# Kernel optimization log

Hardware: AMD Instinct MI355X
Metric: run time of the kernel (lower is better)

Reference implementation:

```python
import jax, jax.numpy as jnp
import numpy as np

HARD_NUM = 700      # hardcoded self.hard_num in HardOIMLoss
OIM_SCALAR = 30.0   # oim_scalar init arg
N, D, P, Q = 4096, 256, 5532, 5000


def _l2norm(x):
    return x / jnp.linalg.norm(x, axis=-1, keepdims=True)


def setup_inputs() -> dict:
    key = jax.random.key(0)
    k1, k2, k3, k4, k5 = jax.random.split(key, 5)
    # OIM features and lookup tables are L2-normalized rows
    inputs = _l2norm(jax.random.normal(k1, (N, D), dtype=jnp.float32))
    lut = _l2norm(jax.random.normal(k2, (P, D), dtype=jnp.float32))
    cq = _l2norm(jax.random.normal(k3, (Q, D), dtype=jnp.float32))
    reliability = jax.random.uniform(k4, (P + Q,), dtype=jnp.float32)
    labels = jax.random.randint(k5, (N,), 0, P, dtype=jnp.int32)
    return {"inputs": inputs, "labels": labels, "lut": lut, "cq": cq,
            "reliability": reliability}


def reference(inputs, labels, lut, cq, reliability):
    # projected[n, c] = <inputs_n, table_c> * reliability_c ;  table = [lut; cq]
    table = jnp.concatenate([lut, cq], axis=0)            # [P+Q, D]
    projected = (inputs @ table.T) * reliability[None, :]  # [N, P+Q]
    C = projected.shape[1]
    # value at sorted-descending index HARD_NUM == (HARD_NUM+1)-th largest
    boundary = jax.lax.top_k(projected, HARD_NUM + 1)[0][:, -1]  # [N]
    hard_mask = projected >= boundary[:, None]
    label_mask = jnp.arange(C, dtype=labels.dtype)[None, :] == labels[:, None]
    mask = hard_mask | label_mask
    logits = jnp.where(mask, projected * OIM_SCALAR, -jnp.inf)
    # cross entropy (mean over rows); label column is always unmasked
    logZ = jax.scipy.special.logsumexp(logits, axis=1)
    tgt = jnp.take_along_axis(logits, labels[:, None].astype(jnp.int32), axis=1)[:, 0]
    return jnp.mean(logZ - tgt)
```

## Files before the change

### kernel.cpp

```cpp
#include <hip/hip_runtime.h>
#include <math.h>

#define N_ROWS 4096
#define DIM    256
#define P_SZ   5532
#define Q_SZ   5000
#define C_COLS 10532
#define TPAD   10624
#define PSTR   10624
#define NGR    (PSTR / 8)
#define NDW    (PSTR / 4)
#define K_SEL  701
#define SCALAR 30.0f
#define C2     (SCALAR * 1.4426950408889634f)

typedef __attribute__((ext_vector_type(8))) short   short8;
typedef __attribute__((ext_vector_type(4))) float   float4_t;
typedef __attribute__((ext_vector_type(4))) unsigned short ushort4_t;
typedef __attribute__((ext_vector_type(8))) unsigned short ushort8_t;
typedef __attribute__((ext_vector_type(4))) unsigned int  uint4_t;

__device__ __forceinline__ unsigned short f2bf(float f) {
    unsigned u = __float_as_uint(f);
    unsigned r = u + 0x7FFFu + ((u >> 16) & 1u);
    return (unsigned short)(r >> 16);
}
__device__ __forceinline__ float bf2f(unsigned short u) {
    return __uint_as_float((unsigned)u << 16);
}
__device__ __forceinline__ unsigned short key16(unsigned short u) {
    return (u & 0x8000u) ? (unsigned short)(~u) : (unsigned short)(u | 0x8000u);
}
__device__ __forceinline__ float key2f16(unsigned key) {
    unsigned short b = (key & 0x8000u) ? (unsigned short)(key & 0x7FFFu)
                                       : (unsigned short)(~key & 0xFFFFu);
    return bf2f(b);
}
__device__ __forceinline__ void gload16(const void* g, void* l) {
    __builtin_amdgcn_global_load_lds(
        (const __attribute__((address_space(1))) unsigned int*)g,
        (__attribute__((address_space(3))) unsigned int*)l, 16, 0, 0);
}

#define NIN_G  (N_ROWS * DIM / 4)
#define NTAB_G (TPAD * DIM / 4)

__global__ __launch_bounds__(256) void convert_bf16(
    const float* __restrict__ inputs, const float* __restrict__ lut,
    const float* __restrict__ cq, unsigned short* __restrict__ in_bf,
    unsigned short* __restrict__ tab_bf)
{
    const int g = blockIdx.x * 256 + threadIdx.x;
    if (g >= NIN_G + NTAB_G) return;
    float4_t v;
    unsigned short* dst;
    if (g < NIN_G) {
        v = *(const float4_t*)&inputs[(size_t)g * 4];
        dst = in_bf + (size_t)g * 4;
    } else {
        const int t = g - NIN_G;
        const int row = t >> 6;
        const int c4  = (t & 63) * 4;
        if (row < P_SZ)        v = *(const float4_t*)&lut[(size_t)row * DIM + c4];
        else if (row < C_COLS) v = *(const float4_t*)&cq[(size_t)(row - P_SZ) * DIM + c4];
        else                   v = (float4_t){0.f, 0.f, 0.f, 0.f};
        dst = tab_bf + (size_t)t * 4;
    }
    ushort4_t h = { f2bf(v.x), f2bf(v.y), f2bf(v.z), f2bf(v.w) };
    *(ushort4_t*)dst = h;
}

#define NWG_X 83
#define NWG_Y 32
#define NWG   (NWG_X * NWG_Y)
#define CSTR  132

__global__ __launch_bounds__(256) void gemm_proj(
    const unsigned short* __restrict__ in_bf,
    const unsigned short* __restrict__ tab_bf,
    const float* __restrict__ rel,
    unsigned short* __restrict__ proj)
{
    __shared__ __align__(16) unsigned short smem[128 * CSTR];
    unsigned short* At = smem;
    unsigned short* Bt = smem + 128 * 64;

    const int tid  = threadIdx.x;
    const int lane = tid & 63, wid = tid >> 6;
    const int wm = wid >> 1, wn = wid & 1;

    const int phys = blockIdx.x;
    const int wg   = (phys & 7) * (NWG / 8) + (phys >> 3);
    const int bx   = wg >> 5;
    const int by   = wg & 31;
    const int row0 = by * 128, col0 = bx * 128;

    float4_t acc[4][4];
    #pragma unroll
    for (int i = 0; i < 4; ++i)
        #pragma unroll
        for (int j = 0; j < 4; ++j)
            acc[i][j] = (float4_t){0.f, 0.f, 0.f, 0.f};

    for (int k0 = 0; k0 < DIM; k0 += 64) {
        #pragma unroll
        for (int it = 0; it < 4; ++it) {
            const int g  = it * 256 + tid;
            const int r  = g >> 3;
            const int kb = ((g & 7) * 16) ^ ((r & 7) << 4);
            gload16(in_bf  + (size_t)(row0 + r) * DIM + k0 + (kb >> 1),
                    (char*)At + g * 16);
            gload16(tab_bf + (size_t)(col0 + r) * DIM + k0 + (kb >> 1),
                    (char*)Bt + g * 16);
        }
        __syncthreads();

        #pragma unroll
        for (int kk = 0; kk < 2; ++kk) {
            const int krow = lane & 15;
            const int kb   = kk * 64 + ((lane >> 4) << 4);
            short8 af[4], bfr[4];
            #pragma unroll
            for (int i = 0; i < 4; ++i) {
                const int r = wm * 64 + i * 16 + krow;
                af[i] = *(const short8*)((const char*)At + (r * 128 + (kb ^ ((r & 7) << 4))));
            }
            #pragma unroll
            for (int j = 0; j < 4; ++j) {
                const int r = wn * 64 + j * 16 + krow;
                bfr[j] = *(const short8*)((const char*)Bt + (r * 128 + (kb ^ ((r & 7) << 4))));
            }
            #pragma unroll
            for (int i = 0; i < 4; ++i)
                #pragma unroll
                for (int j = 0; j < 4; ++j)
                    acc[i][j] = __builtin_amdgcn_mfma_f32_16x16x32_bf16(af[i], bfr[j], acc[i][j], 0, 0, 0);
        }
        __syncthreads();
    }

    const int lr = (lane >> 4) << 2;
    const int lc = lane & 15;
    #pragma unroll
    for (int j = 0; j < 4; ++j) {
        const int cl  = wn * 64 + j * 16 + lc;
        const int col = col0 + cl;
        const bool pad = (col >= C_COLS);
        const float rl = pad ? 0.f : rel[col];
        #pragma unroll
        for (int i = 0; i < 4; ++i) {
            const int rbase = wm * 64 + i * 16 + lr;
            #pragma unroll
            for (int rr = 0; rr < 4; ++rr)
                smem[(rbase + rr) * CSTR + cl] =
                    pad ? (unsigned short)0u : key16(f2bf(acc[i][j][rr] * rl));
        }
    }
    __syncthreads();
    #pragma unroll
    for (int it = 0; it < 8; ++it) {
        const int g = it * 256 + tid;
        const int r = g >> 4;
        const int c8 = (g & 15) * 8;
        *(ushort8_t*)(proj + (size_t)(row0 + r) * PSTR + col0 + c8) =
            *(const ushort8_t*)&smem[r * CSTR + c8];
    }
}

#define NCPY 16
__global__ __launch_bounds__(256) void row_loss_kernel(
    const unsigned short* __restrict__ proj, const int* __restrict__ labels,
    float* __restrict__ row_loss)
{
    __shared__ unsigned h1[NCPY * 257];
    __shared__ unsigned h2[256];
    __shared__ unsigned wsum[4];
    __shared__ float    fsum[4];
    __shared__ unsigned sel_bin, sel_k, sel_sub;

    const int tid = threadIdx.x, lane = tid & 63, wid = tid >> 6;
    const int row = blockIdx.x;
    const uint4_t* prow = (const uint4_t*)(proj + (size_t)row * PSTR);
    const unsigned cbase = (unsigned)(tid & (NCPY - 1)) * 257;

    for (int i = tid; i < NCPY * 257; i += 256) h1[i] = 0;
    if (tid < 256) h2[tid] = 0;
    __syncthreads();

    #pragma unroll
    for (int it = 0; it < 5; ++it) {
        const uint4_t w = prow[it * 256 + tid];
        #pragma unroll
        for (int d = 0; d < 4; ++d) {
            atomicAdd(&h1[cbase + ((w[d] >> 8) & 0xFFu)], 1u);
            atomicAdd(&h1[cbase + (w[d] >> 24)], 1u);
        }
    }
    if (tid < NGR - 1280) {
        const uint4_t w = prow[1280 + tid];
        #pragma unroll
        for (int d = 0; d < 4; ++d) {
            atomicAdd(&h1[cbase + ((w[d] >> 8) & 0xFFu)], 1u);
            atomicAdd(&h1[cbase + (w[d] >> 24)], 1u);
        }
    }
    __syncthreads();

    {
        unsigned c = 0;
        #pragma unroll
        for (int cp = 0; cp < NCPY; ++cp) c += h1[cp * 257 + tid];
        unsigned incl = c;
        #pragma unroll
        for (int off = 1; off < 64; off <<= 1) {
            const unsigned t = __shfl_down(incl, off, 64);
            if (lane + off < 64) incl += t;
        }
        if (lane == 0) wsum[wid] = incl;
        __syncthreads();
        unsigned above = incl - c;
        for (int w = wid + 1; w < 4; ++w) above += wsum[w];
        if (above < K_SEL && above + c >= K_SEL) {
            sel_bin = (unsigned)tid; sel_k = K_SEL - above;
        }
    }
    __syncthreads();
    const unsigned b1 = sel_bin;
    const unsigned k2 = sel_k;
    __syncthreads();

    #pragma unroll
    for (int it = 0; it < 5; ++it) {
        const uint4_t w = prow[it * 256 + tid];
        #pragma unroll
        for (int d = 0; d < 4; ++d) {
            const unsigned lo = w[d] & 0xFFFFu, hi = w[d] >> 16;
            if ((lo >> 8) == b1) atomicAdd(&h2[lo & 0xFFu], 1u);
            if ((hi >> 8) == b1) atomicAdd(&h2[hi & 0xFFu], 1u);
        }
    }
    if (tid < NGR - 1280) {
        const uint4_t w = prow[1280 + tid];
        #pragma unroll
        for (int d = 0; d < 4; ++d) {
            const unsigned lo = w[d] & 0xFFFFu, hi = w[d] >> 16;
            if ((lo >> 8) == b1) atomicAdd(&h2[lo & 0xFFu], 1u);
            if ((hi >> 8) == b1) atomicAdd(&h2[hi & 0xFFu], 1u);
        }
    }
    __syncthreads();

    {
        const unsigned c = h2[tid];
        unsigned incl = c;
        #pragma unroll
        for (int off = 1; off < 64; off <<= 1) {
            const unsigned t = __shfl_down(incl, off, 64);
            if (lane + off < 64) incl += t;
        }
        if (lane == 0) wsum[wid] = incl;
        __syncthreads();
        unsigned above = incl - c;
        for (int w = wid + 1; w < 4; ++w) above += wsum[w];
        if (above < k2 && above + c >= k2) sel_sub = (unsigned)tid;
    }
    __syncthreads();
    const unsigned bkey = (b1 << 8) | sel_sub;

    float s = 0.f;
    #pragma unroll
    for (int it = 0; it < 5; ++it) {
        const uint4_t w = prow[it * 256 + tid];
        #pragma unroll
        for (int d = 0; d < 4; ++d) {
            const unsigned lo = w[d] & 0xFFFFu, hi = w[d] >> 16;
            if (lo >= bkey) s += exp2f(C2 * key2f16(lo) - C2);
            if (hi >= bkey) s += exp2f(C2 * key2f16(hi) - C2);
        }
    }
    if (tid < NGR - 1280) {
        const uint4_t w = prow[1280 + tid];
        #pragma unroll
        for (int d = 0; d < 4; ++d) {
            const unsigned lo = w[d] & 0xFFFFu, hi = w[d] >> 16;
            if (lo >= bkey) s += exp2f(C2 * key2f16(lo) - C2);
            if (hi >= bkey) s += exp2f(C2 * key2f16(hi) - C2);
        }
    }
    #pragma unroll
    for (int off = 1; off < 64; off <<= 1) {
        const float t = __shfl_down(s, off, 64);
        if (lane + off < 64) s += t;
    }
    if (lane == 0) fsum[wid] = s;
    __syncthreads();

    if (tid == 0) {
        float total = fsum[0] + fsum[1] + fsum[2] + fsum[3];
        const unsigned ulk = ((const unsigned short*)prow)[labels[row]];
        const float pl = key2f16(ulk);
        if (ulk < bkey) total += exp2f(C2 * pl - C2);
        row_loss[row] = SCALAR * 1.0f + logf(total) - SCALAR * pl;
    }
}

__global__ __launch_bounds__(256) void final_reduce(
    const float* __restrict__ row_loss, float* __restrict__ out)
{
    __shared__ float fred[4];
    const int tid = threadIdx.x, lane = tid & 63, wid = tid >> 6;
    float s = 0.f;
    for (int i = tid; i < N_ROWS; i += 256) s += row_loss[i];
    #pragma unroll
    for (int off = 1; off < 64; off <<= 1) {
        const float t = __shfl_down(s, off, 64);
        if (lane + off < 64) s += t;
    }
    if (lane == 0) fred[wid] = s;
    __syncthreads();
    if (tid == 0) out[0] = (fred[0] + fred[1] + fred[2] + fred[3]) / (float)N_ROWS;
}

extern "C" void kernel_launch(void* const* d_in, const int* in_sizes, int n_in,
                              void* d_out, int out_size, void* d_ws, size_t ws_size,
                              hipStream_t stream) {
    const float* inputs = (const float*)d_in[0];
    const int*   labels = (const int*)d_in[1];
    const float* lut    = (const float*)d_in[2];
    const float* cq     = (const float*)d_in[3];
    const float* rel    = (const float*)d_in[4];
    float* out = (float*)d_out;

    unsigned short* in_bf  = (unsigned short*)d_ws;
    unsigned short* tab_bf = in_bf  + (size_t)N_ROWS * DIM;
    unsigned short* proj   = tab_bf + (size_t)TPAD * DIM;
    float* rl_buf = (float*)(proj + (size_t)N_ROWS * PSTR);

    convert_bf16<<<(NIN_G + NTAB_G) / 256, 256, 0, stream>>>(inputs, lut, cq, in_bf, tab_bf);
    gemm_proj<<<NWG, 256, 0, stream>>>(in_bf, tab_bf, rel, proj);
    row_loss_kernel<<<N_ROWS, 256, 0, stream>>>(proj, labels, rl_buf);
    final_reduce<<<1, 256, 0, stream>>>(rl_buf, out);
}
```

Before: 97.59 us.

## Double-buffer GEMM K-loop and cache row data in registers for loss passes

The GEMM now double-buffers A/B tiles in shared memory, issuing the next K-slice's async loads before computing the current one. It uses explicit vmcnt waits and raw barriers to overlap global loads with MFMA work. The row-loss kernel loads each row's data into registers once and reuses it for all three passes instead of re-reading global memory, doubles the histogram copies, and merges duplicate bin increments. The trade-off is more registers and shared memory, which may lower occupancy.

```diff
diff --git a/kernel.cpp b/kernel.cpp
--- a/kernel.cpp
+++ b/kernel.cpp
@@ -8,8 +8,7 @@
 #define C_COLS 10532
 #define TPAD   10624
 #define PSTR   10624
-#define NGR    (PSTR / 8)
-#define NDW    (PSTR / 4)
+#define NGR    (PSTR / 16)
 #define K_SEL  701
 #define SCALAR 30.0f
 #define C2     (SCALAR * 1.4426950408889634f)
@@ -81,9 +80,7 @@
     const float* __restrict__ rel,
     unsigned short* __restrict__ proj)
 {
-    __shared__ __align__(16) unsigned short smem[128 * CSTR];
-    unsigned short* At = smem;
-    unsigned short* Bt = smem + 128 * 64;
+    __shared__ __align__(16) unsigned short smem[4][128 * 64];
 
     const int tid  = threadIdx.x;
     const int lane = tid & 63, wid = tid >> 6;
@@ -102,19 +99,32 @@
         for (int j = 0; j < 4; ++j)
             acc[i][j] = (float4_t){0.f, 0.f, 0.f, 0.f};
 
-    for (int k0 = 0; k0 < DIM; k0 += 64) {
+    auto STAGE = [&](int b, int k0) {
         #pragma unroll
         for (int it = 0; it < 4; ++it) {
             const int g  = it * 256 + tid;
             const int r  = g >> 3;
             const int kb = ((g & 7) * 16) ^ ((r & 7) << 4);
             gload16(in_bf  + (size_t)(row0 + r) * DIM + k0 + (kb >> 1),
-                    (char*)At + g * 16);
+                    (char*)&smem[b][0] + g * 16);
             gload16(tab_bf + (size_t)(col0 + r) * DIM + k0 + (kb >> 1),
-                    (char*)Bt + g * 16);
-        }
-        __syncthreads();
-
+                    (char*)&smem[2 + b][0] + g * 16);
+        }
+    };
+
+    STAGE(0, 0);
+    #pragma unroll
+    for (int t = 0; t < 4; ++t) {
+        if (t < 3) {
+            STAGE((t + 1) & 1, (t + 1) * 64);
+            asm volatile("s_waitcnt vmcnt(8)" ::: "memory");
+        } else {
+            asm volatile("s_waitcnt vmcnt(0)" ::: "memory");
+        }
+        __builtin_amdgcn_s_barrier();
+
+        const char* At = (const char*)&smem[t & 1][0];
+        const char* Bt = (const char*)&smem[2 + (t & 1)][0];
         #pragma unroll
         for (int kk = 0; kk < 2; ++kk) {
             const int krow = lane & 15;
@@ -123,12 +133,12 @@
             #pragma unroll
             for (int i = 0; i < 4; ++i) {
                 const int r = wm * 64 + i * 16 + krow;
-                af[i] = *(const short8*)((const char*)At + (r * 128 + (kb ^ ((r & 7) << 4))));
+                af[i] = *(const short8*)(At + (r * 128 + (kb ^ ((r & 7) << 4))));
             }
             #pragma unroll
             for (int j = 0; j < 4; ++j) {
                 const int r = wn * 64 + j * 16 + krow;
-                bfr[j] = *(const short8*)((const char*)Bt + (r * 128 + (kb ^ ((r & 7) << 4))));
+                bfr[j] = *(const short8*)(Bt + (r * 128 + (kb ^ ((r & 7) << 4))));
             }
             #pragma unroll
             for (int i = 0; i < 4; ++i)
@@ -136,9 +146,10 @@
                 for (int j = 0; j < 4; ++j)
                     acc[i][j] = __builtin_amdgcn_mfma_f32_16x16x32_bf16(af[i], bfr[j], acc[i][j], 0, 0, 0);
         }
-        __syncthreads();
-    }
-
+        __builtin_amdgcn_s_barrier();
+    }
+
+    unsigned short* ctile = &smem[0][0];
     const int lr = (lane >> 4) << 2;
     const int lc = lane & 15;
     #pragma unroll
@@ -152,7 +163,7 @@
             const int rbase = wm * 64 + i * 16 + lr;
             #pragma unroll
             for (int rr = 0; rr < 4; ++rr)
-                smem[(rbase + rr) * CSTR + cl] =
+                ctile[(rbase + rr) * CSTR + cl] =
                     pad ? (unsigned short)0u : key16(f2bf(acc[i][j][rr] * rl));
         }
     }
@@ -163,11 +174,11 @@
         const int r = g >> 4;
         const int c8 = (g & 15) * 8;
         *(ushort8_t*)(proj + (size_t)(row0 + r) * PSTR + col0 + c8) =
-            *(const ushort8_t*)&smem[r * CSTR + c8];
-    }
-}
-
-#define NCPY 16
+            *(const ushort8_t*)&ctile[r * CSTR + c8];
+    }
+}
+
+#define NCPY 32
 __global__ __launch_bounds__(256) void row_loss_kernel(
     const unsigned short* __restrict__ proj, const int* __restrict__ labels,
     float* __restrict__ row_loss)
@@ -183,26 +194,38 @@
     const uint4_t* prow = (const uint4_t*)(proj + (size_t)row * PSTR);
     const unsigned cbase = (unsigned)(tid & (NCPY - 1)) * 257;
 
-    for (int i = tid; i < NCPY * 257; i += 256) h1[i] = 0;
-    if (tid < 256) h2[tid] = 0;
-    __syncthreads();
-
-    #pragma unroll
-    for (int it = 0; it < 5; ++it) {
-        const uint4_t w = prow[it * 256 + tid];
-        #pragma unroll
-        for (int d = 0; d < 4; ++d) {
-            atomicAdd(&h1[cbase + ((w[d] >> 8) & 0xFFu)], 1u);
-            atomicAdd(&h1[cbase + (w[d] >> 24)], 1u);
-        }
-    }
-    if (tid < NGR - 1280) {
-        const uint4_t w = prow[1280 + tid];
-        #pragma unroll
-        for (int d = 0; d < 4; ++d) {
-            atomicAdd(&h1[cbase + ((w[d] >> 8) & 0xFFu)], 1u);
-            atomicAdd(&h1[cbase + (w[d] >> 24)], 1u);
-        }
+    #pragma unroll
+    for (int i = 0; i < NCPY * 257; i += 256)
+        if (i + tid < NCPY * 257) h1[i + tid] = 0;
+    h2[tid] = 0;
+    __syncthreads();
+
+    const int tailv = (1280 + tid < NGR);
+    uint4_t r0 = prow[tid];
+    uint4_t r1 = prow[256 + tid];
+    uint4_t r2 = prow[512 + tid];
+    uint4_t r3 = prow[768 + tid];
+    uint4_t r4 = prow[1024 + tid];
+    uint4_t r5 = prow[tailv ? 1280 + tid : 1279];
+
+    auto HB = [&](unsigned w) {
+        const unsigned bl = (w >> 8) & 0xFFu, bh = w >> 24;
+        if (bl == bh) atomicAdd(&h1[cbase + bl], 2u);
+        else { atomicAdd(&h1[cbase + bl], 1u); atomicAdd(&h1[cbase + bh], 1u); }
+    };
+    #pragma unroll
+    for (int d = 0; d < 4; ++d) HB(r0[d]);
+    #pragma unroll
+    for (int d = 0; d < 4; ++d) HB(r1[d]);
+    #pragma unroll
+    for (int d = 0; d < 4; ++d) HB(r2[d]);
+    #pragma unroll
+    for (int d = 0; d < 4; ++d) HB(r3[d]);
+    #pragma unroll
+    for (int d = 0; d < 4; ++d) HB(r4[d]);
+    if (tailv) {
+        #pragma unroll
+        for (int d = 0; d < 4; ++d) HB(r5[d]);
     }
     __syncthreads();
 
@@ -229,24 +252,24 @@
     const unsigned k2 = sel_k;
     __syncthreads();
 
-    #pragma unroll
-    for (int it = 0; it < 5; ++it) {
-        const uint4_t w = prow[it * 256 + tid];
-        #pragma unroll
-        for (int d = 0; d < 4; ++d) {
-            const unsigned lo = w[d] & 0xFFFFu, hi = w[d] >> 16;
-            if ((lo >> 8) == b1) atomicAdd(&h2[lo & 0xFFu], 1u);
-            if ((hi >> 8) == b1) atomicAdd(&h2[hi & 0xFFu], 1u);
-        }
-    }
-    if (tid < NGR - 1280) {
-        const uint4_t w = prow[1280 + tid];
-        #pragma unroll
-        for (int d = 0; d < 4; ++d) {
-            const unsigned lo = w[d] & 0xFFFFu, hi = w[d] >> 16;
-            if ((lo >> 8) == b1) atomicAdd(&h2[lo & 0xFFu], 1u);
-            if ((hi >> 8) == b1) atomicAdd(&h2[hi & 0xFFu], 1u);
-        }
+    auto SB = [&](unsigned w) {
+        const unsigned lo = w & 0xFFFFu, hi = w >> 16;
+        if ((lo >> 8) == b1) atomicAdd(&h2[lo & 0xFFu], 1u);
+        if ((hi >> 8) == b1) atomicAdd(&h2[hi & 0xFFu], 1u);
+    };
+    #pragma unroll
+    for (int d = 0; d < 4; ++d) SB(r0[d]);
+    #pragma unroll
+    for (int d = 0; d < 4; ++d) SB(r1[d]);
+    #pragma unroll
+    for (int d = 0; d < 4; ++d) SB(r2[d]);
+    #pragma unroll
+    for (int d = 0; d < 4; ++d) SB(r3[d]);
+    #pragma unroll
+    for (int d = 0; d < 4; ++d) SB(r4[d]);
+    if (tailv) {
+        #pragma unroll
+        for (int d = 0; d < 4; ++d) SB(r5[d]);
     }
     __syncthreads();
 
@@ -268,24 +291,24 @@
     const unsigned bkey = (b1 << 8) | sel_sub;
 
     float s = 0.f;
-    #pragma unroll
-    for (int it = 0; it < 5; ++it) {
-        const uint4_t w = prow[it * 256 + tid];
-        #pragma unroll
-        for (int d = 0; d < 4; ++d) {
-            const unsigned lo = w[d] & 0xFFFFu, hi = w[d] >> 16;
-            if (lo >= bkey) s += exp2f(C2 * key2f16(lo) - C2);
-            if (hi >= bkey) s += exp2f(C2 * key2f16(hi) - C2);
-        }
-    }
-    if (tid < NGR - 1280) {
-        const uint4_t w = prow[1280 + tid];
-        #pragma unroll
-        for (int d = 0; d < 4; ++d) {
-            const unsigned lo = w[d] & 0xFFFFu, hi = w[d] >> 16;
-            if (lo >= bkey) s += exp2f(C2 * key2f16(lo) - C2);
-            if (hi >= bkey) s += exp2f(C2 * key2f16(hi) - C2);
-        }
+    auto EX = [&](unsigned w) {
+        const unsigned lo = w & 0xFFFFu, hi = w >> 16;
+        if (lo >= bkey) s += exp2f(C2 * key2f16(lo) - C2);
+        if (hi >= bkey) s += exp2f(C2 * key2f16(hi) - C2);
+    };
+    #pragma unroll
+    for (int d = 0; d < 4; ++d) EX(r0[d]);
+    #pragma unroll
+    for (int d = 0; d < 4; ++d) EX(r1[d]);
+    #pragma unroll
+    for (int d = 0; d < 4; ++d) EX(r2[d]);
+    #pragma unroll
+    for (int d = 0; d < 4; ++d) EX(r3[d]);
+    #pragma unroll
+    for (int d = 0; d < 4; ++d) EX(r4[d]);
+    if (tailv) {
+        #pragma unroll
+        for (int d = 0; d < 4; ++d) EX(r5[d]);
     }
     #pragma unroll
     for (int off = 1; off < 64; off <<= 1) {
```

After: 105.1 us. 7.7% more time.

## Keep projected row in registers and stash candidates in LDS for later passes

Applied to the files above, without the earlier changes.

The row-loss kernel now loads each row's bf16 keys into registers once instead of re-reading global memory in three passes. After the coarse histogram, each thread stashes the keys at or above the selected coarse bin into shared memory (up to 32 per thread). The fine histogram and the exp-sum then iterate only over those stashed candidates, with a fallback to a full register scan if any thread overflows its stash. This adds about 16KB of LDS and more live registers, which may lower occupancy.

```diff
diff --git a/kernel.cpp b/kernel.cpp
--- a/kernel.cpp
+++ b/kernel.cpp
@@ -8,8 +8,7 @@
 #define C_COLS 10532
 #define TPAD   10624
 #define PSTR   10624
-#define NGR    (PSTR / 8)
-#define NDW    (PSTR / 4)
+#define NGR    (PSTR / 16)
 #define K_SEL  701
 #define SCALAR 30.0f
 #define C2     (SCALAR * 1.4426950408889634f)
@@ -167,16 +166,18 @@
     }
 }
 
-#define NCPY 16
+#define NCPY  16
+#define SCAP  32
 __global__ __launch_bounds__(256) void row_loss_kernel(
     const unsigned short* __restrict__ proj, const int* __restrict__ labels,
     float* __restrict__ row_loss)
 {
     __shared__ unsigned h1[NCPY * 257];
+    __shared__ unsigned short stash[SCAP * 256];
     __shared__ unsigned h2[256];
     __shared__ unsigned wsum[4];
     __shared__ float    fsum[4];
-    __shared__ unsigned sel_bin, sel_k, sel_sub;
+    __shared__ unsigned sel_bin, sel_k, sel_sub, ovf;
 
     const int tid = threadIdx.x, lane = tid & 63, wid = tid >> 6;
     const int row = blockIdx.x;
@@ -184,25 +185,35 @@
     const unsigned cbase = (unsigned)(tid & (NCPY - 1)) * 257;
 
     for (int i = tid; i < NCPY * 257; i += 256) h1[i] = 0;
-    if (tid < 256) h2[tid] = 0;
-    __syncthreads();
-
-    #pragma unroll
-    for (int it = 0; it < 5; ++it) {
-        const uint4_t w = prow[it * 256 + tid];
-        #pragma unroll
-        for (int d = 0; d < 4; ++d) {
-            atomicAdd(&h1[cbase + ((w[d] >> 8) & 0xFFu)], 1u);
-            atomicAdd(&h1[cbase + (w[d] >> 24)], 1u);
-        }
-    }
-    if (tid < NGR - 1280) {
-        const uint4_t w = prow[1280 + tid];
-        #pragma unroll
-        for (int d = 0; d < 4; ++d) {
-            atomicAdd(&h1[cbase + ((w[d] >> 8) & 0xFFu)], 1u);
-            atomicAdd(&h1[cbase + (w[d] >> 24)], 1u);
-        }
+    h2[tid] = 0;
+    if (tid == 0) ovf = 0;
+    __syncthreads();
+
+    const int tailv = (1280 + tid < NGR);
+    uint4_t r0 = prow[tid];
+    uint4_t r1 = prow[256 + tid];
+    uint4_t r2 = prow[512 + tid];
+    uint4_t r3 = prow[768 + tid];
+    uint4_t r4 = prow[1024 + tid];
+    uint4_t r5 = prow[tailv ? 1280 + tid : 1279];
+
+    auto HB = [&](unsigned w) {
+        atomicAdd(&h1[cbase + ((w >> 8) & 0xFFu)], 1u);
+        atomicAdd(&h1[cbase + (w >> 24)], 1u);
+    };
+    #pragma unroll
+    for (int d = 0; d < 4; ++d) HB(r0[d]);
+    #pragma unroll
+    for (int d = 0; d < 4; ++d) HB(r1[d]);
+    #pragma unroll
+    for (int d = 0; d < 4; ++d) HB(r2[d]);
+    #pragma unroll
+    for (int d = 0; d < 4; ++d) HB(r3[d]);
+    #pragma unroll
+    for (int d = 0; d < 4; ++d) HB(r4[d]);
+    if (tailv) {
+        #pragma unroll
+        for (int d = 0; d < 4; ++d) HB(r5[d]);
     }
     __syncthreads();
 
@@ -227,66 +238,96 @@
     __syncthreads();
     const unsigned b1 = sel_bin;
     const unsigned k2 = sel_k;
-    __syncthreads();
-
-    #pragma unroll
-    for (int it = 0; it < 5; ++it) {
-        const uint4_t w = prow[it * 256 + tid];
-        #pragma unroll
-        for (int d = 0; d < 4; ++d) {
-            const unsigned lo = w[d] & 0xFFFFu, hi = w[d] >> 16;
+    const unsigned kfloor = b1 << 8;
+    __syncthreads();
+
+    unsigned cnt = 0;
+    auto ST = [&](unsigned key) {
+        if (key >= kfloor) {
+            if (cnt < SCAP) stash[cnt * 256 + tid] = (unsigned short)key;
+            else ovf = 1u;
+            ++cnt;
+        }
+    };
+    auto SW = [&](uint4_t w) {
+        #pragma unroll
+        for (int d = 0; d < 4; ++d) { ST(w[d] & 0xFFFFu); ST(w[d] >> 16); }
+    };
+    SW(r0); SW(r1); SW(r2); SW(r3); SW(r4);
+    if (tailv) SW(r5);
+    __syncthreads();
+
+    float s = 0.f;
+    unsigned bkey;
+    if (ovf == 0) {
+        const unsigned kceil = kfloor + 256u;
+        for (unsigned c = 0; c < cnt; ++c) {
+            const unsigned key = stash[c * 256 + tid];
+            if (key < kceil) atomicAdd(&h2[key & 0xFFu], 1u);
+        }
+        __syncthreads();
+        {
+            const unsigned c = h2[tid];
+            unsigned incl = c;
+            #pragma unroll
+            for (int off = 1; off < 64; off <<= 1) {
+                const unsigned t = __shfl_down(incl, off, 64);
+                if (lane + off < 64) incl += t;
+            }
+            if (lane == 0) wsum[wid] = incl;
+            __syncthreads();
+            unsigned above = incl - c;
+            for (int w = wid + 1; w < 4; ++w) above += wsum[w];
+            if (above < k2 && above + c >= k2) sel_sub = (unsigned)tid;
+        }
+        __syncthreads();
+        bkey = kfloor | sel_sub;
+        for (unsigned c = 0; c < cnt; ++c) {
+            const unsigned key = stash[c * 256 + tid];
+            if (key >= bkey) s += exp2f(C2 * key2f16(key) - C2);
+        }
+    } else {
+        auto SB = [&](unsigned w) {
+            const unsigned lo = w & 0xFFFFu, hi = w >> 16;
             if ((lo >> 8) == b1) atomicAdd(&h2[lo & 0xFFu], 1u);
             if ((hi >> 8) == b1) atomicAdd(&h2[hi & 0xFFu], 1u);
-        }
-    }
-    if (tid < NGR - 1280) {
-        const uint4_t w = prow[1280 + tid];
-        #pragma unroll
-        for (int d = 0; d < 4; ++d) {
-            const unsigned lo = w[d] & 0xFFFFu, hi = w[d] >> 16;
-            if ((lo >> 8) == b1) atomicAdd(&h2[lo & 0xFFu], 1u);
-            if ((hi >> 8) == b1) atomicAdd(&h2[hi & 0xFFu], 1u);
-        }
-    }
-    __syncthreads();
-
-    {
-        const unsigned c = h2[tid];
-        unsigned incl = c;
-        #pragma unroll
-        for (int off = 1; off < 64; off <<= 1) {
-            const unsigned t = __shfl_down(incl, off, 64);
-            if (lane + off < 64) incl += t;
-        }
-        if (lane == 0) wsum[wid] = incl;
-        __syncthreads();
-        unsigned above = incl - c;
-        for (int w = wid + 1; w < 4; ++w) above += wsum[w];
-        if (above < k2 && above + c >= k2) sel_sub = (unsigned)tid;
-    }
-    __syncthreads();
-    const unsigned bkey = (b1 << 8) | sel_sub;
-
-    float s = 0.f;
-    #pragma unroll
-    for (int it = 0; it < 5; ++it) {
-        const uint4_t w = prow[it * 256 + tid];
-        #pragma unroll
-        for (int d = 0; d < 4; ++d) {
-            const unsigned lo = w[d] & 0xFFFFu, hi = w[d] >> 16;
+        };
+        SB(r0[0]); SB(r0[1]); SB(r0[2]); SB(r0[3]);
+        SB(r1[0]); SB(r1[1]); SB(r1[2]); SB(r1[3]);
+        SB(r2[0]); SB(r2[1]); SB(r2[2]); SB(r2[3]);
+        SB(r3[0]); SB(r3[1]); SB(r3[2]); SB(r3[3]);
+        SB(r4[0]); SB(r4[1]); SB(r4[2]); SB(r4[3]);
+        if (tailv) { SB(r5[0]); SB(r5[1]); SB(r5[2]); SB(r5[3]); }
+        __syncthreads();
+        {
+            const unsigned c = h2[tid];
+            unsigned incl = c;
+            #pragma unroll
+            for (int off = 1; off < 64; off <<= 1) {
+                const unsigned t = __shfl_down(incl, off, 64);
+                if (lane + off < 64) incl += t;
+            }
+            if (lane == 0) wsum[wid] = incl;
+            __syncthreads();
+            unsigned above = incl - c;
+            for (int w = wid + 1; w < 4; ++w) above += wsum[w];
+            if (above < k2 && above + c >= k2) sel_sub = (unsigned)tid;
+        }
+        __syncthreads();
+        bkey = kfloor | sel_sub;
+        auto EX = [&](unsigned w) {
+            const unsigned lo = w & 0xFFFFu, hi = w >> 16;
             if (lo >= bkey) s += exp2f(C2 * key2f16(lo) - C2);
             if (hi >= bkey) s += exp2f(C2 * key2f16(hi) - C2);
-        }
-    }
-    if (tid < NGR - 1280) {
-        const uint4_t w = prow[1280 + tid];
-        #pragma unroll
-        for (int d = 0; d < 4; ++d) {
-            const unsigned lo = w[d] & 0xFFFFu, hi = w[d] >> 16;
-            if (lo >= bkey) s += exp2f(C2 * key2f16(lo) - C2);
-            if (hi >= bkey) s += exp2f(C2 * key2f16(hi) - C2);
-        }
-    }
+        };
+        EX(r0[0]); EX(r0[1]); EX(r0[2]); EX(r0[3]);
+        EX(r1[0]); EX(r1[1]); EX(r1[2]); EX(r1[3]);
+        EX(r2[0]); EX(r2[1]); EX(r2[2]); EX(r2[3]);
+        EX(r3[0]); EX(r3[1]); EX(r3[2]); EX(r3[3]);
+        EX(r4[0]); EX(r4[1]); EX(r4[2]); EX(r4[3]);
+        if (tailv) { EX(r5[0]); EX(r5[1]); EX(r5[2]); EX(r5[3]); }
+    }
+
     #pragma unroll
     for (int off = 1; off < 64; off <<= 1) {
         const float t = __shfl_down(s, off, 64);
```

After: 100.2 us. 2.6% more time.
